# Kernel optimization log

Measured on AMD Instinct MI355X. Metric: run time of the kernel, lower is better.

Reference implementation:

```python
import jax, jax.numpy as jnp
import numpy as np

BW = 31      # band width = 2*banded_matrix_width + 1
SCALE = 4    # weight_scale_factor


def setup_inputs() -> dict:
    key = jax.random.key(0)
    k1, k2 = jax.random.split(key)
    # pre_weights: [n_psfs, (h//SCALE)*(w//SCALE), BW]
    pre_weights = jax.random.normal(k1, (32, 4096, 31), dtype=jnp.float32) * 0.1
    # x: [b, c, h, w]
    x = jax.random.normal(k2, (4, 8, 256, 256), dtype=jnp.float32)
    return {"pre_weights": pre_weights, "x": x}


def reference(pre_weights, x):
    bw = BW
    b, c, h, w = x.shape
    pad = bw // 2
    # F.pad(x, (pad, pad)) pads only the last (width) dim
    xp = jnp.pad(x, ((0, 0), (0, 0), (0, 0), (pad, pad)))
    # F.unfold with kernel (1, bw): sliding windows along width -> [b, c, h, w, bw]
    win = jnp.stack([xp[..., k:k + w] for k in range(bw)], axis=-1)
    x_unf = win.reshape(b * c, h * w, bw)  # [bc, hw, bw]

    n = pre_weights.shape[0]
    d = h // SCALE
    # reshape to [n, d, d, bw] and bilinearly upsample spatial dims to (h, w)
    # (matches F.interpolate mode='bilinear', align_corners=False)
    wgt = pre_weights.reshape(n, d, d, bw)
    wgt = jax.image.resize(wgt, (n, h, w, bw), method='bilinear')
    wgt = wgt.reshape(n, h * w, bw)  # [n, hw, bw]

    # per-pixel banded contraction: [bc, hw, bw] x [n, hw, bw] -> [bc, n, hw]
    out = jnp.einsum('bpd,npd->bnp', x_unf, wgt)
    return out.reshape(b * c, n, h, w)
```

## Files before the change

kernel.cpp:

```cpp
#include <hip/hip_runtime.h>
#include <hip/hip_bf16.h>

#define Dd   64
#define BWk  31
#define NTH  256
#define NS   32
#define CS   (32 * NS)
#define NCOL 18
#define RS   64

typedef float  f32x4   __attribute__((ext_vector_type(4)));
typedef short  bf16x8  __attribute__((ext_vector_type(8)));
typedef float  float4a __attribute__((ext_vector_type(4), aligned(4)));

__device__ __forceinline__ unsigned pk2(float lo, float hi) {
    __hip_bfloat162 h = __float22bfloat162_rn(make_float2(lo, hi));
    union { __hip_bfloat162 h; unsigned u; } c; c.h = h; return c.u;
}

__device__ __forceinline__ void lds_barrier() {
    asm volatile("s_waitcnt lgkmcnt(0)" ::: "memory");
    __builtin_amdgcn_s_barrier();
    __builtin_amdgcn_sched_barrier(0);
}

__global__ __launch_bounds__(NTH, 3)
void band_mfma(const float* __restrict__ pw,
               const float* __restrict__ x,
               float* __restrict__ out)
{
    __shared__ unsigned short wYb[NCOL * CS];
    __shared__ float tile[2][32 * RS];

    const int tid = threadIdx.x;
    const int bx  = blockIdx.x;
    const int y   = blockIdx.y;
    const int x0  = bx * 64;

    const int yq = y >> 2, ry = y & 3;
    const int y0i = yq + ((ry < 2) ? -1 : 0);
    const float fy = 0.125f + 0.25f * (float)((ry + 2) & 3);
    const int y0c = (y0i < 0) ? 0 : y0i;
    const int y1c = (y0i + 1 > Dd - 1) ? Dd - 1 : (y0i + 1);
    const int cxb = (x0 >> 2) - 1;

    {
        const int n  = tid >> 3;
        const int k0 = (tid & 7) << 2;
        const bool lastk = (k0 == 28);
        const size_t rb0 = ((size_t)n * 4096) * BWk + k0;
        #pragma unroll 6
        for (int i = 0; i < NCOL; ++i) {
            int cx = cxb + i;
            cx = (cx < 0) ? 0 : ((cx > Dd - 1) ? Dd - 1 : cx);
            const size_t rb = rb0 + (size_t)cx * BWk;
            float4a a = *(const float4a*)(pw + rb + (size_t)y0c * (Dd * BWk));
            float4a b = *(const float4a*)(pw + rb + (size_t)y1c * (Dd * BWk));
            float v0 = fmaf(fy, b.x - a.x, a.x);
            float v1 = fmaf(fy, b.y - a.y, a.y);
            float v2 = fmaf(fy, b.z - a.z, a.z);
            float v3 = lastk ? 0.f : fmaf(fy, b.w - a.w, a.w);
            *(uint2*)&wYb[i * CS + n * NS + k0] = make_uint2(pk2(v0, v1), pk2(v2, v3));
        }
    }
    __syncthreads();

    const int lane = tid & 63;
    const int px   = lane & 15;
    const int q    = lane >> 4;
    const int t    = tid >> 6;
    const int xt0  = x0 + 16 * t;

    bf16x8 A[6][2];
    #pragma unroll
    for (int j = 0; j < 6; ++j) {
        const unsigned short* base = &wYb[(4 * t + j) * CS + q * 8];
        A[j][0] = *(const bf16x8*)&base[px * NS];
        A[j][1] = *(const bf16x8*)&base[(16 + px) * NS];
    }

    const int rx = px & 3;
    const float fx = 0.125f + 0.25f * (float)((rx + 2) & 3);
    const int j0 = (px >> 2) + ((rx < 2) ? 0 : 1);
    float c[6];
    #pragma unroll
    for (int j = 0; j < 6; ++j)
        c[j] = (j == j0) ? (1.f - fx) : ((j == j0 + 1) ? fx : 0.f);

    const int gxb = xt0 + px + q * 8 - 15;
    const bool edge = (bx == 0 && t == 0) || (bx == 3 && t == 3);
    const f32x4 zero = {0.f, 0.f, 0.f, 0.f};

    const int rr = lane >> 4;
    const int ii = lane & 15;
    const size_t sb = (size_t)y * 256 + (size_t)x0 + (size_t)(ii * 4);

    #pragma unroll 2
    for (int bc = 0; bc < 32; ++bc) {
        const float* xrow = x + ((size_t)bc * 256 + y) * 256;

        float4a v0, v1;
        if (!edge) {
            v0 = *(const float4a*)(xrow + gxb);
            v1 = *(const float4a*)(xrow + gxb + 4);
        } else {
            float tv[8];
            #pragma unroll
            for (int i = 0; i < 8; ++i) {
                int gx = gxb + i;
                tv[i] = ((unsigned)gx < 256u) ? xrow[gx] : 0.f;
            }
            v0 = *(float4a*)&tv[0]; v1 = *(float4a*)&tv[4];
        }
        union { unsigned u[4]; bf16x8 v; } bb;
        bb.u[0] = pk2(v0.x, v0.y);
        bb.u[1] = pk2(v0.z, v0.w);
        bb.u[2] = pk2(v1.x, v1.y);
        bb.u[3] = pk2(v1.z, v1.w);
        const bf16x8 B = bb.v;

        float* tl = tile[bc & 1];
        #pragma unroll
        for (int mh = 0; mh < 2; ++mh) {
            f32x4 acc = zero;
            #pragma unroll
            for (int j = 0; j < 6; ++j) {
                f32x4 g = __builtin_amdgcn_mfma_f32_16x16x32_bf16(
                              A[j][mh], B, zero, 0, 0, 0);
                acc += g * c[j];
            }
            float* w = tl + (mh * 16 + q * 4) * RS + 16 * t + px;
            w[0]      = acc.x;
            w[RS]     = acc.y;
            w[2 * RS] = acc.z;
            w[3 * RS] = acc.w;
        }
        lds_barrier();

        const float* ts = tile[bc & 1];
        #pragma unroll
        for (int s = 0; s < 2; ++s) {
            const int row = t * 8 + s * 4 + rr;
            f32x4 v = *(const f32x4*)&ts[row * RS + ii * 4];
            f32x4* dst = (f32x4*)(out + (size_t)(bc * 32 + row) * 65536 + sb);
            __builtin_nontemporal_store(v, dst);
        }
    }
}

extern "C" void kernel_launch(void* const* d_in, const int* in_sizes, int n_in,
                              void* d_out, int out_size, void* d_ws, size_t ws_size,
                              hipStream_t stream) {
    const float* pw = (const float*)d_in[0];
    const float* x  = (const float*)d_in[1];
    float* out = (float*)d_out;

    dim3 grid(4, 256, 1);
    dim3 block(NTH, 1, 1);
    band_mfma<<<grid, block, 0, stream>>>(pw, x, out);
}
```

Baseline: 79.53 us.

## Stage interpolated weights in four LDS passes to shrink shared memory and raise occupancy

The weight staging buffer shrinks from holding all 32 PSFs to 8 at a time. The prologue now loops four times, each pass filling the smaller buffer and letting half the lanes pull their A fragments, with two barriers per pass. The smaller LDS footprint lets launch bounds rise from 3 to 6 blocks per CU, which is meant to hide the latency of the global loads and output stores. The cost is eight barriers in the prologue instead of one, and tighter register limits that could cause spills given the 12 bf16x8 A fragments held per thread.

```diff
diff --git a/kernel.cpp b/kernel.cpp
--- a/kernel.cpp
+++ b/kernel.cpp
@@ -4,9 +4,7 @@
 #define Dd   64
 #define BWk  31
 #define NTH  256
-#define NS   32
-#define CS   (32 * NS)
-#define NCOL 18
+#define CS   256
 #define RS   64
 
 typedef float  f32x4   __attribute__((ext_vector_type(4)));
@@ -24,12 +22,12 @@
     __builtin_amdgcn_sched_barrier(0);
 }
 
-__global__ __launch_bounds__(NTH, 3)
+__global__ __launch_bounds__(NTH, 6)
 void band_mfma(const float* __restrict__ pw,
                const float* __restrict__ x,
                float* __restrict__ out)
 {
-    __shared__ unsigned short wYb[NCOL * CS];
+    __shared__ unsigned short wYb[18 * CS];
     __shared__ float tile[2][32 * RS];
 
     const int tid = threadIdx.x;
@@ -44,27 +42,6 @@
     const int y1c = (y0i + 1 > Dd - 1) ? Dd - 1 : (y0i + 1);
     const int cxb = (x0 >> 2) - 1;
 
-    {
-        const int n  = tid >> 3;
-        const int k0 = (tid & 7) << 2;
-        const bool lastk = (k0 == 28);
-        const size_t rb0 = ((size_t)n * 4096) * BWk + k0;
-        #pragma unroll 6
-        for (int i = 0; i < NCOL; ++i) {
-            int cx = cxb + i;
-            cx = (cx < 0) ? 0 : ((cx > Dd - 1) ? Dd - 1 : cx);
-            const size_t rb = rb0 + (size_t)cx * BWk;
-            float4a a = *(const float4a*)(pw + rb + (size_t)y0c * (Dd * BWk));
-            float4a b = *(const float4a*)(pw + rb + (size_t)y1c * (Dd * BWk));
-            float v0 = fmaf(fy, b.x - a.x, a.x);
-            float v1 = fmaf(fy, b.y - a.y, a.y);
-            float v2 = fmaf(fy, b.z - a.z, a.z);
-            float v3 = lastk ? 0.f : fmaf(fy, b.w - a.w, a.w);
-            *(uint2*)&wYb[i * CS + n * NS + k0] = make_uint2(pk2(v0, v1), pk2(v2, v3));
-        }
-    }
-    __syncthreads();
-
     const int lane = tid & 63;
     const int px   = lane & 15;
     const int q    = lane >> 4;
@@ -72,11 +49,40 @@
     const int xt0  = x0 + 16 * t;
 
     bf16x8 A[6][2];
-    #pragma unroll
-    for (int j = 0; j < 6; ++j) {
-        const unsigned short* base = &wYb[(4 * t + j) * CS + q * 8];
-        A[j][0] = *(const bf16x8*)&base[px * NS];
-        A[j][1] = *(const bf16x8*)&base[(16 + px) * NS];
+    {
+        const int kq  = tid & 7;
+        const int k0  = kq << 2;
+        const int cg  = (tid >> 3) & 3;
+        const int n_l = tid >> 5;
+        const bool lastk = (kq == 7);
+        #pragma unroll
+        for (int p = 0; p < 4; ++p) {
+            const int n_g = p * 8 + n_l;
+            const size_t rb0 = ((size_t)n_g * 4096) * BWk + k0;
+            #pragma unroll
+            for (int ci = cg; ci < 18; ci += 4) {
+                int cx = cxb + ci;
+                cx = (cx < 0) ? 0 : ((cx > Dd - 1) ? Dd - 1 : cx);
+                const size_t rb = rb0 + (size_t)cx * BWk;
+                float4a a = *(const float4a*)(pw + rb + (size_t)y0c * (Dd * BWk));
+                float4a b = *(const float4a*)(pw + rb + (size_t)y1c * (Dd * BWk));
+                float v0 = fmaf(fy, b.x - a.x, a.x);
+                float v1 = fmaf(fy, b.y - a.y, a.y);
+                float v2 = fmaf(fy, b.z - a.z, a.z);
+                float v3 = lastk ? 0.f : fmaf(fy, b.w - a.w, a.w);
+                *(uint2*)&wYb[ci * CS + n_l * 32 + k0] =
+                    make_uint2(pk2(v0, v1), pk2(v2, v3));
+            }
+            __syncthreads();
+            if ((px >> 3) == (p & 1)) {
+                const int mh = p >> 1;
+                #pragma unroll
+                for (int j = 0; j < 6; ++j)
+                    A[j][mh] = *(const bf16x8*)
+                        &wYb[(4 * t + j) * CS + (px & 7) * 32 + q * 8];
+            }
+            __syncthreads();
+        }
     }
 
     const int rx = px & 3;
```

Measured after the change: 214.4 us. +169.6%, slower.
